# Optimization experiments

Measured on AMD Instinct MI355X. Metric: run time of the kernel, lower is better.

## Reference

```python
import jax, jax.numpy as jnp
import numpy as np

KEEP_P = 0.75  # 1 - dropout_p, dropout_p = 0.25

def setup_inputs() -> dict:
    key = jax.random.key(0)
    k1, k2, k3, k4 = jax.random.split(key, 4)
    B, Sq, Skv, D, Dv = 8, 2048, 2048, 128, 128
    x1 = jax.random.normal(k1, (B, Sq, D), dtype=jnp.float32)
    x2 = jax.random.normal(k2, (B, Skv, D), dtype=jnp.float32)
    x3 = jax.random.normal(k3, (B, Skv, Dv), dtype=jnp.float32)
    # torch Dropout(p): mask = bernoulli(keep_p) / keep_p
    keep = jax.random.bernoulli(k4, KEEP_P, (B, Sq, Skv))
    dropout_mask = keep.astype(jnp.float32) / KEEP_P
    return {"x1": x1, "x2": x2, "x3": x3, "dropout_mask": dropout_mask}

def reference(x1, x2, x3, dropout_mask):
    # scores: [B, Sq, Skv] = x1 @ x2^T (no scale: scale_factor is None)
    scores = jnp.einsum("bqd,bkd->bqk", x1, x2)
    probs = jax.nn.softmax(scores, axis=-1)
    probs = probs * dropout_mask  # dropout with fixed mask
    out = jnp.einsum("bqk,bkv->bqv", probs, x3)  # [B, Sq, Dv]
    return out
```

## Files before the change

### kernel.cpp

```cpp
#include <hip/hip_runtime.h>
#include <stdint.h>

#define SQ 2048
#define SKV 2048
#define DD 128
#define NB 8
#define M0 40.0f
#define KEEP_INV 1.3333333333333333f

typedef float    f4v __attribute__((ext_vector_type(4)));
typedef __bf16   bf4 __attribute__((ext_vector_type(4)));
typedef __bf16   bf8 __attribute__((ext_vector_type(8)));
typedef _Float16 h8  __attribute__((ext_vector_type(8)));

__device__ __forceinline__ void async16(const void* g, void* l) {
    __builtin_amdgcn_global_load_lds(
        (const __attribute__((address_space(1))) void*)g,
        (__attribute__((address_space(3))) void*)l, 16, 0, 0);
}

__global__ void cast_f16_swz(const float* __restrict__ src,
                             _Float16* __restrict__ dst) {
    int tid = blockIdx.x * 256 + threadIdx.x;
    int d8 = tid & 15;
    int kv = (tid >> 4) & (SKV - 1);
    int b  = tid >> 15;
    const float* p = src + ((size_t)b * SKV + kv) * DD + d8 * 8;
    f4v a0 = *(const f4v*)p;
    f4v a1 = *(const f4v*)(p + 4);
    h8 h;
#pragma unroll
    for (int c = 0; c < 4; c++) {
        h[c]     = (_Float16)a0[c];
        h[c + 4] = (_Float16)a1[c];
    }
    int s = d8 >> 2, g = d8 & 3, kb32 = kv >> 5, row = kv & 31;
    *(h8*)(dst + (size_t)(b * 64 + kb32) * 4096 + (size_t)((s * 32 + row) * 4 + g) * 8) = h;
}

__global__ void transpose_v_swz(const float* __restrict__ v, __bf16* __restrict__ vtf) {
    __shared__ __bf16 tile[32][33];
    int kb32 = blockIdx.x, dv0 = blockIdx.y * 32, b = blockIdx.z;
    int tx = threadIdx.x, ty = threadIdx.y;
    const float* src = v + ((size_t)b * SKV + kb32 * 32 + ty) * DD + dv0 + tx;
#pragma unroll
    for (int i = 0; i < 32; i += 8)
        tile[ty + i][tx] = (__bf16)src[(size_t)i * DD];
    __syncthreads();
    int pcol = (tx < 16) ? ((tx >> 2) << 3) + (tx & 3)
                         : (((tx - 16) >> 2) << 3) + 4 + (tx & 3);
    __bf16* dst = vtf + (size_t)(b * 64 + kb32) * 4096 + pcol;
#pragma unroll
    for (int i = 0; i < 32; i += 8)
        dst[(size_t)(dv0 + ty + i) * 32] = tile[tx][ty + i];
}

__global__ __launch_bounds__(256, 4) void attn_kernel(
    const float* __restrict__ Qf, const _Float16* __restrict__ Kh,
    const __bf16* __restrict__ Vt, const float* __restrict__ mask,
    float* __restrict__ O_part, float* __restrict__ l_part,
    int nsp, int kv_len) {
    __shared__ __align__(16) char smem[2][16384];
    const int lin = blockIdx.x;
    const int per_xcd = (NB * nsp) >> 3;
    const int xcd = lin & 7;
    const int idx = lin >> 3;
    const int slice = xcd * per_xcd + (idx >> 5);
    const int qblk = idx & 31;
    const int b = slice / nsp, sid = slice % nsp;
    const int tid = threadIdx.x;
    const int w = tid >> 6, lane = tid & 63;
    const int g = lane >> 4, n = lane & 15;
    const int qb = qblk * 64 + w * 16;
    const int kv0 = sid * kv_len;
    const int kb32_0 = kv0 >> 5;
    const int niter = kv_len >> 5;

    const float* Qrow = Qf + ((size_t)b * SQ + qb + n) * DD + g * 8;
    h8 qf[4];
#pragma unroll
    for (int s = 0; s < 4; s++) {
        f4v v0 = *(const f4v*)(Qrow + s * 32);
        f4v v1 = *(const f4v*)(Qrow + s * 32 + 4);
#pragma unroll
        for (int c = 0; c < 4; c++) {
            qf[s][c]     = (_Float16)v0[c];
            qf[s][c + 4] = (_Float16)v1[c];
        }
    }

    const _Float16* Kt0 = Kh + (size_t)(b * 64 + kb32_0) * 4096;
    const __bf16*   Vt0 = Vt + (size_t)(b * 64 + kb32_0) * 4096;
    auto stage = [&](int buf, int it) {
#pragma unroll
        for (int jj = 0; jj < 4; jj++) {
            int j = w * 4 + jj;
            if (j < 8)
                async16(Kt0 + (size_t)it * 4096 + j * 512 + lane * 8,
                        (void*)&smem[buf][j * 1024]);
            else
                async16(Vt0 + (size_t)it * 4096 + (j - 8) * 512 + lane * 8,
                        (void*)&smem[buf][8192 + (j - 8) * 1024]);
        }
    };

    const float* mrow = mask + ((size_t)b * SQ + qb + n) * SKV + kv0;
    stage(0, 0);
    f4v mc0 = __builtin_nontemporal_load((const f4v*)(mrow + g * 4));
    f4v mc1 = __builtin_nontemporal_load((const f4v*)(mrow + 16 + g * 4));

    const f4v zero = {0.f, 0.f, 0.f, 0.f};
    f4v o_acc[8];
#pragma unroll
    for (int t = 0; t < 8; t++) o_acc[t] = zero;
    float l_run = 0.f;

    for (int it = 0; it < niter; it++) {
        __syncthreads();
        f4v mn0, mn1;
        if (it + 1 < niter) {
            stage((it + 1) & 1, it + 1);
            mn0 = __builtin_nontemporal_load(
                (const f4v*)(mrow + (it + 1) * 32 + g * 4));
            mn1 = __builtin_nontemporal_load(
                (const f4v*)(mrow + (it + 1) * 32 + 16 + g * 4));
        }

        const _Float16* Lk = (const _Float16*)smem[it & 1];
        const __bf16*   Lv = (const __bf16*)(smem[it & 1] + 8192);

        f4v sa0 = zero, sa1 = zero;
#pragma unroll
        for (int s = 0; s < 4; s++) {
            h8 a0 = *(const h8*)(Lk + (size_t)((s * 32 + n) * 4 + g) * 8);
            h8 a1 = *(const h8*)(Lk + (size_t)((s * 32 + n + 16) * 4 + g) * 8);
            sa0 = __builtin_amdgcn_mfma_f32_16x16x32_f16(a0, qf[s], sa0, 0, 0, 0);
            sa1 = __builtin_amdgcn_mfma_f32_16x16x32_f16(a1, qf[s], sa1, 0, 0, 0);
        }

        float p0e[4], p1e[4];
#pragma unroll
        for (int r = 0; r < 4; r++) {
            p0e[r] = __expf(sa0[r] - M0);
            p1e[r] = __expf(sa1[r] - M0);
            l_run += p0e[r] + p1e[r];
        }
        bf8 pf;
#pragma unroll
        for (int j = 0; j < 4; j++) {
            pf[j]     = (mc0[j] > 0.5f) ? (__bf16)p0e[j] : (__bf16)0.0f;
            pf[j + 4] = (mc1[j] > 0.5f) ? (__bf16)p1e[j] : (__bf16)0.0f;
        }

#pragma unroll
        for (int t = 0; t < 8; t++) {
            bf8 vf = *(const bf8*)(Lv + (size_t)((t * 16 + n) * 4 + g) * 8);
            o_acc[t] = __builtin_amdgcn_mfma_f32_16x16x32_bf16(pf, vf, o_acc[t], 0, 0, 0);
        }
        if (it + 1 < niter) { mc0 = mn0; mc1 = mn1; }
    }

    l_run += __shfl_xor(l_run, 16);
    l_run += __shfl_xor(l_run, 32);
    const int tile = (b * 128 + qblk * 4 + w) * nsp + sid;
    float* op = O_part + (size_t)tile * 2048;
#pragma unroll
    for (int t = 0; t < 8; t++)
#pragma unroll
        for (int r = 0; r < 4; r++)
            op[(g * 4 + r) * 128 + t * 16 + n] = o_acc[t][r];
    if (g == 0) l_part[(size_t)tile * 16 + n] = l_run;
}

__global__ __launch_bounds__(256) void combine_kernel(
    const float* __restrict__ O_part, const float* __restrict__ l_part,
    float* __restrict__ out, int nsp) {
    const int qt = blockIdx.x;
    const int b  = blockIdx.y;
    const int tbase = (b * 128 + qt) * nsp;
    const int q  = threadIdx.x >> 4;
    const int d8 = threadIdx.x & 15;
    f4v a0 = {0.f, 0.f, 0.f, 0.f}, a1 = {0.f, 0.f, 0.f, 0.f};
    float L = 0.f;
    for (int s = 0; s < nsp; s++) {
        const float* op = O_part + (size_t)(tbase + s) * 2048 + q * 128 + d8 * 8;
        a0 += *(const f4v*)op;
        a1 += *(const f4v*)(op + 4);
        L  += l_part[(size_t)(tbase + s) * 16 + q];
    }
    float scale = KEEP_INV / L;
    float* o = out + ((size_t)b * SQ + qt * 16 + q) * DD + d8 * 8;
    *(f4v*)o       = a0 * scale;
    *(f4v*)(o + 4) = a1 * scale;
}

extern "C" void kernel_launch(void* const* d_in, const int* in_sizes, int n_in,
                              void* d_out, int out_size, void* d_ws, size_t ws_size,
                              hipStream_t stream) {
    const float* x1   = (const float*)d_in[0];
    const float* x2   = (const float*)d_in[1];
    const float* x3   = (const float*)d_in[2];
    const float* mask = (const float*)d_in[3];
    float* out = (float*)d_out;

    const size_t kelems = (size_t)NB * SKV * DD;
    _Float16* Kh  = (_Float16*)d_ws;
    __bf16*   VTf = (__bf16*)(Kh + kelems);
    float*    O_part = (float*)(VTf + kelems);

    size_t base = 2 * kelems * 2;
    size_t per  = (size_t)NB * 128 * (2048 + 16) * sizeof(float);
    int nsp = 4;
    while (nsp > 1 && base + (size_t)nsp * per > ws_size) nsp >>= 1;
    float* l_part = O_part + (size_t)NB * 128 * nsp * 2048;

    hipLaunchKernelGGL(cast_f16_swz, dim3(NB * SKV * 16 / 256), dim3(256), 0, stream,
                       x2, Kh);
    hipLaunchKernelGGL(transpose_v_swz, dim3(SKV / 32, DD / 32, NB), dim3(32, 8), 0,
                       stream, x3, VTf);
    hipLaunchKernelGGL(attn_kernel, dim3(32 * NB * nsp), dim3(256), 0, stream,
                       x1, Kh, VTf, mask, O_part, l_part, nsp, SKV / nsp);
    hipLaunchKernelGGL(combine_kernel, dim3(128, NB), dim3(256), 0, stream,
                       O_part, l_part, out, nsp);
}
```

Baseline: 238.3 us.

## Process two query subtiles per wave to reuse K/V LDS reads, double KV split

Each wave now handles 32 query rows (two 16-row subtiles) instead of 16, so each block covers 128 queries and every K/V fragment read from LDS feeds two MFMAs. The KV split count rises from 4 to 8 to keep the grid large, and launch bounds drop to 3 blocks per CU to leave room for the doubled accumulators. This cuts LDS traffic and staging per query, but raises register pressure and doubles the partial-output traffic that the combine kernel must read.

```diff
diff --git a/kernel.cpp b/kernel.cpp
--- a/kernel.cpp
+++ b/kernel.cpp
@@ -7,6 +7,7 @@
 #define NB 8
 #define M0 40.0f
 #define KEEP_INV 1.3333333333333333f
+#define NSP 8
 
 typedef float    f4v __attribute__((ext_vector_type(4)));
 typedef __bf16   bf4 __attribute__((ext_vector_type(4)));
@@ -55,7 +56,7 @@
         dst[(size_t)(dv0 + ty + i) * 32] = tile[tx][ty + i];
 }
 
-__global__ __launch_bounds__(256, 4) void attn_kernel(
+__global__ __launch_bounds__(256, 3) void attn_kernel(
     const float* __restrict__ Qf, const _Float16* __restrict__ Kh,
     const __bf16* __restrict__ Vt, const float* __restrict__ mask,
     float* __restrict__ O_part, float* __restrict__ l_part,
@@ -65,27 +66,30 @@
     const int per_xcd = (NB * nsp) >> 3;
     const int xcd = lin & 7;
     const int idx = lin >> 3;
-    const int slice = xcd * per_xcd + (idx >> 5);
-    const int qblk = idx & 31;
+    const int slice = xcd * per_xcd + (idx >> 4);
+    const int qblk = idx & 15;
     const int b = slice / nsp, sid = slice % nsp;
     const int tid = threadIdx.x;
     const int w = tid >> 6, lane = tid & 63;
     const int g = lane >> 4, n = lane & 15;
-    const int qb = qblk * 64 + w * 16;
+    const int qb = qblk * 128 + w * 32;
     const int kv0 = sid * kv_len;
     const int kb32_0 = kv0 >> 5;
     const int niter = kv_len >> 5;
 
-    const float* Qrow = Qf + ((size_t)b * SQ + qb + n) * DD + g * 8;
-    h8 qf[4];
-#pragma unroll
-    for (int s = 0; s < 4; s++) {
-        f4v v0 = *(const f4v*)(Qrow + s * 32);
-        f4v v1 = *(const f4v*)(Qrow + s * 32 + 4);
-#pragma unroll
-        for (int c = 0; c < 4; c++) {
-            qf[s][c]     = (_Float16)v0[c];
-            qf[s][c + 4] = (_Float16)v1[c];
+    h8 qf[2][4];
+#pragma unroll
+    for (int u = 0; u < 2; u++) {
+        const float* Qrow = Qf + ((size_t)b * SQ + qb + u * 16 + n) * DD + g * 8;
+#pragma unroll
+        for (int s = 0; s < 4; s++) {
+            f4v v0 = *(const f4v*)(Qrow + s * 32);
+            f4v v1 = *(const f4v*)(Qrow + s * 32 + 4);
+#pragma unroll
+            for (int c = 0; c < 4; c++) {
+                qf[u][s][c]     = (_Float16)v0[c];
+                qf[u][s][c + 4] = (_Float16)v1[c];
+            }
         }
     }
 
@@ -104,72 +108,91 @@
         }
     };
 
-    const float* mrow = mask + ((size_t)b * SQ + qb + n) * SKV + kv0;
+    const float* mrow0 = mask + ((size_t)b * SQ + qb + n) * SKV + kv0;
+    const float* mrow1 = mrow0 + (size_t)16 * SKV;
     stage(0, 0);
-    f4v mc0 = __builtin_nontemporal_load((const f4v*)(mrow + g * 4));
-    f4v mc1 = __builtin_nontemporal_load((const f4v*)(mrow + 16 + g * 4));
+    f4v mc[2][2], mn[2][2];
+    mc[0][0] = __builtin_nontemporal_load((const f4v*)(mrow0 + g * 4));
+    mc[0][1] = __builtin_nontemporal_load((const f4v*)(mrow0 + 16 + g * 4));
+    mc[1][0] = __builtin_nontemporal_load((const f4v*)(mrow1 + g * 4));
+    mc[1][1] = __builtin_nontemporal_load((const f4v*)(mrow1 + 16 + g * 4));
 
     const f4v zero = {0.f, 0.f, 0.f, 0.f};
-    f4v o_acc[8];
-#pragma unroll
-    for (int t = 0; t < 8; t++) o_acc[t] = zero;
-    float l_run = 0.f;
+    f4v o_acc[2][8];
+#pragma unroll
+    for (int u = 0; u < 2; u++)
+#pragma unroll
+        for (int t = 0; t < 8; t++) o_acc[u][t] = zero;
+    float l_run[2] = {0.f, 0.f};
 
     for (int it = 0; it < niter; it++) {
         __syncthreads();
-        f4v mn0, mn1;
         if (it + 1 < niter) {
             stage((it + 1) & 1, it + 1);
-            mn0 = __builtin_nontemporal_load(
-                (const f4v*)(mrow + (it + 1) * 32 + g * 4));
-            mn1 = __builtin_nontemporal_load(
-                (const f4v*)(mrow + (it + 1) * 32 + 16 + g * 4));
+            const int o = (it + 1) * 32;
+            mn[0][0] = __builtin_nontemporal_load((const f4v*)(mrow0 + o + g * 4));
+            mn[0][1] = __builtin_nontemporal_load((const f4v*)(mrow0 + o + 16 + g * 4));
+            mn[1][0] = __builtin_nontemporal_load((const f4v*)(mrow1 + o + g * 4));
+            mn[1][1] = __builtin_nontemporal_load((const f4v*)(mrow1 + o + 16 + g * 4));
         }
 
         const _Float16* Lk = (const _Float16*)smem[it & 1];
         const __bf16*   Lv = (const __bf16*)(smem[it & 1] + 8192);
 
-        f4v sa0 = zero, sa1 = zero;
+        f4v sa[2][2];
+#pragma unroll
+        for (int u = 0; u < 2; u++) { sa[u][0] = zero; sa[u][1] = zero; }
 #pragma unroll
         for (int s = 0; s < 4; s++) {
             h8 a0 = *(const h8*)(Lk + (size_t)((s * 32 + n) * 4 + g) * 8);
             h8 a1 = *(const h8*)(Lk + (size_t)((s * 32 + n + 16) * 4 + g) * 8);
-            sa0 = __builtin_amdgcn_mfma_f32_16x16x32_f16(a0, qf[s], sa0, 0, 0, 0);
-            sa1 = __builtin_amdgcn_mfma_f32_16x16x32_f16(a1, qf[s], sa1, 0, 0, 0);
-        }
-
-        float p0e[4], p1e[4];
-#pragma unroll
-        for (int r = 0; r < 4; r++) {
-            p0e[r] = __expf(sa0[r] - M0);
-            p1e[r] = __expf(sa1[r] - M0);
-            l_run += p0e[r] + p1e[r];
-        }
-        bf8 pf;
-#pragma unroll
-        for (int j = 0; j < 4; j++) {
-            pf[j]     = (mc0[j] > 0.5f) ? (__bf16)p0e[j] : (__bf16)0.0f;
-            pf[j + 4] = (mc1[j] > 0.5f) ? (__bf16)p1e[j] : (__bf16)0.0f;
+#pragma unroll
+            for (int u = 0; u < 2; u++) {
+                sa[u][0] = __builtin_amdgcn_mfma_f32_16x16x32_f16(a0, qf[u][s], sa[u][0], 0, 0, 0);
+                sa[u][1] = __builtin_amdgcn_mfma_f32_16x16x32_f16(a1, qf[u][s], sa[u][1], 0, 0, 0);
+            }
+        }
+
+        bf8 pf[2];
+#pragma unroll
+        for (int u = 0; u < 2; u++) {
+#pragma unroll
+            for (int r = 0; r < 4; r++) {
+                float p0 = __expf(sa[u][0][r] - M0);
+                float p1 = __expf(sa[u][1][r] - M0);
+                l_run[u] += p0 + p1;
+                pf[u][r]     = (mc[u][0][r] > 0.5f) ? (__bf16)p0 : (__bf16)0.0f;
+                pf[u][r + 4] = (mc[u][1][r] > 0.5f) ? (__bf16)p1 : (__bf16)0.0f;
+            }
         }
 
 #pragma unroll
         for (int t = 0; t < 8; t++) {
             bf8 vf = *(const bf8*)(Lv + (size_t)((t * 16 + n) * 4 + g) * 8);
-            o_acc[t] = __builtin_amdgcn_mfma_f32_16x16x32_bf16(pf, vf, o_acc[t], 0, 0, 0);
-        }
-        if (it + 1 < niter) { mc0 = mn0; mc1 = mn1; }
-    }
-
-    l_run += __shfl_xor(l_run, 16);
-    l_run += __shfl_xor(l_run, 32);
-    const int tile = (b * 128 + qblk * 4 + w) * nsp + sid;
-    float* op = O_part + (size_t)tile * 2048;
-#pragma unroll
-    for (int t = 0; t < 8; t++)
-#pragma unroll
-        for (int r = 0; r < 4; r++)
-            op[(g * 4 + r) * 128 + t * 16 + n] = o_acc[t][r];
-    if (g == 0) l_part[(size_t)tile * 16 + n] = l_run;
+#pragma unroll
+            for (int u = 0; u < 2; u++)
+                o_acc[u][t] = __builtin_amdgcn_mfma_f32_16x16x32_bf16(pf[u], vf, o_acc[u][t], 0, 0, 0);
+        }
+        if (it + 1 < niter) {
+#pragma unroll
+            for (int u = 0; u < 2; u++) { mc[u][0] = mn[u][0]; mc[u][1] = mn[u][1]; }
+        }
+    }
+
+#pragma unroll
+    for (int u = 0; u < 2; u++) {
+        float lr = l_run[u];
+        lr += __shfl_xor(lr, 16);
+        lr += __shfl_xor(lr, 32);
+        const int tile = (b * 128 + qblk * 8 + w * 2 + u) * nsp + sid;
+        float* op = O_part + (size_t)tile * 2048;
+#pragma unroll
+        for (int t = 0; t < 8; t++)
+#pragma unroll
+            for (int r = 0; r < 4; r++)
+                op[(g * 4 + r) * 128 + t * 16 + n] = o_acc[u][t][r];
+        if (g == 0) l_part[(size_t)tile * 16 + n] = lr;
+    }
 }
 
 __global__ __launch_bounds__(256) void combine_kernel(
@@ -210,7 +233,7 @@
 
     size_t base = 2 * kelems * 2;
     size_t per  = (size_t)NB * 128 * (2048 + 16) * sizeof(float);
-    int nsp = 4;
+    int nsp = NSP;
     while (nsp > 1 && base + (size_t)nsp * per > ws_size) nsp >>= 1;
     float* l_part = O_part + (size_t)NB * 128 * nsp * 2048;
 
@@ -218,7 +241,7 @@
                        x2, Kh);
     hipLaunchKernelGGL(transpose_v_swz, dim3(SKV / 32, DD / 32, NB), dim3(32, 8), 0,
                        stream, x3, VTf);
-    hipLaunchKernelGGL(attn_kernel, dim3(32 * NB * nsp), dim3(256), 0, stream,
+    hipLaunchKernelGGL(attn_kernel, dim3(16 * NB * nsp), dim3(256), 0, stream,
                        x1, Kh, VTf, mask, O_part, l_part, nsp, SKV / nsp);
     hipLaunchKernelGGL(combine_kernel, dim3(128, NB), dim3(256), 0, stream,
                        O_part, l_part, out, nsp);
```

Measured after the change: 290.2 us. 21.8% more time.
